# Kernel optimization log

Hardware: AMD Instinct MI355X
Metric: run time of the kernel (lower is better)

## Reference

```python
import jax, jax.numpy as jnp
import numpy as np
from jax import lax

B, S, MEL, DM, DI, N, K, R, H, V = 2, 2048, 80, 512, 1024, 16, 4, 32, 8, 10000


def setup_inputs() -> dict:
    ks = iter(jax.random.split(jax.random.key(0), 48))
    r = lambda sh, s=0.02: jax.random.normal(next(ks), sh, jnp.float32) * s
    inp = {"mel": jax.random.normal(next(ks), (B, S, MEL), jnp.float32)}
    inp["mel_w"] = r((DM, MEL)); inp["mel_b"] = r((DM,))
    inp["attn_in_w"] = r((3 * DM, DM)); inp["attn_in_b"] = r((3 * DM,))
    inp["attn_out_w"] = r((DM, DM)); inp["attn_out_b"] = r((DM,))
    inp["ln1_g"] = jnp.ones((DM,)); inp["ln1_b"] = jnp.zeros((DM,))
    inp["ln2_g"] = jnp.ones((DM,)); inp["ln2_b"] = jnp.zeros((DM,))
    for p in ("fm", "bm"):
        inp[p + "_in_w"] = r((2 * DI, DM))
        inp[p + "_conv_w"] = r((DI, K), 0.2)
        inp[p + "_conv_b"] = r((DI,), 0.1)
        inp[p + "_x_w"] = r((R + 2 * N, DI))
        inp[p + "_dt_w"] = r((DI, R), 0.1)
        inp[p + "_dt_b"] = r((DI,), 0.1)
        inp[p + "_A_log"] = jnp.log(jnp.tile(jnp.arange(1, N + 1, dtype=jnp.float32), (DI, 1)))
        inp[p + "_D"] = jnp.ones((DI,))
        inp[p + "_out_w"] = r((DM, DI))
    inp["bim_w"] = r((DM, 2 * DM)); inp["bim_b"] = r((DM,))
    inp["out_w"] = r((V, DM)); inp["out_b"] = r((V,))
    return inp


def _ln(x, g, b):
    mu = x.mean(-1, keepdims=True)
    var = ((x - mu) ** 2).mean(-1, keepdims=True)
    return (x - mu) * lax.rsqrt(var + 1e-5) * g + b


def _mha(x, in_w, in_b, out_w, out_b):
    # torch nn.MultiheadAttention default batch_first=False:
    # axis0 = sequence (here the batch dim B), axis1 = batch (here S). Faithful to source.
    L, Nb, E = x.shape
    hd = E // H
    qkv = x @ in_w.T + in_b
    q, k, v = jnp.split(qkv, 3, axis=-1)
    q = q.reshape(L, Nb, H, hd)
    k = k.reshape(L, Nb, H, hd)
    v = v.reshape(L, Nb, H, hd)
    sc = jnp.einsum('lnhd,mnhd->nhlm', q, k) / np.float32(np.sqrt(hd))
    a = jax.nn.softmax(sc, axis=-1)
    o = jnp.einsum('nhlm,mnhd->lnhd', a, v).reshape(L, Nb, E)
    return o @ out_w.T + out_b


def _mamba(x, in_w, conv_w, conv_b, x_w, dt_w, dt_b, A_log, Dp, out_w):
    # mamba_ssm Mamba block: in_proj -> causal depthwise conv + silu -> x_proj ->
    # softplus(dt_proj) -> selective scan -> gate by silu(z) -> out_proj
    Bb, L, _ = x.shape
    xa, z = jnp.split(x @ in_w.T, 2, axis=-1)  # [B,L,DI] each
    xc = lax.conv_general_dilated(xa.transpose(0, 2, 1), conv_w[:, None, :], (1,), [(K - 1, 0)],
                                  dimension_numbers=('NCH', 'OIH', 'NCH'), feature_group_count=DI)
    xc = jax.nn.silu(xc + conv_b[None, :, None]).transpose(0, 2, 1)  # [B,L,DI]
    dbl = xc @ x_w.T  # [B,L,R+2N]
    dt, Bm, Cm = dbl[..., :R], dbl[..., R:R + N], dbl[..., R + N:]
    dt = jax.nn.softplus(dt @ dt_w.T + dt_b)  # [B,L,DI]
    A = -jnp.exp(A_log)  # [DI,N]

    def step(h, ins):
        dt_t, B_t, C_t, x_t = ins  # [B,DI],[B,N],[B,N],[B,DI]
        h = jnp.exp(dt_t[..., None] * A) * h + (dt_t * x_t)[..., None] * B_t[:, None, :]
        return h, jnp.einsum('bdn,bn->bd', h, C_t)

    h0 = jnp.zeros((Bb, DI, N), x.dtype)
    _, ys = lax.scan(step, h0, (dt.transpose(1, 0, 2), Bm.transpose(1, 0, 2),
                                Cm.transpose(1, 0, 2), xc.transpose(1, 0, 2)))
    y = ys.transpose(1, 0, 2) + xc * Dp
    y = y * jax.nn.silu(z)
    return y @ out_w.T


def reference(mel, mel_w, mel_b, attn_in_w, attn_in_b, attn_out_w, attn_out_b,
              ln1_g, ln1_b, ln2_g, ln2_b,
              fm_in_w, fm_conv_w, fm_conv_b, fm_x_w, fm_dt_w, fm_dt_b, fm_A_log, fm_D, fm_out_w,
              bm_in_w, bm_conv_w, bm_conv_b, bm_x_w, bm_dt_w, bm_dt_b, bm_A_log, bm_D, bm_out_w,
              bim_w, bim_b, out_w, out_b):
    x = mel @ mel_w.T + mel_b  # [B,S,DM]
    x = _ln(x + _mha(x, attn_in_w, attn_in_b, attn_out_w, attn_out_b), ln1_g, ln1_b)
    fwd = _mamba(x, fm_in_w, fm_conv_w, fm_conv_b, fm_x_w, fm_dt_w, fm_dt_b, fm_A_log, fm_D, fm_out_w)
    bwd = jnp.flip(_mamba(jnp.flip(x, 1), bm_in_w, bm_conv_w, bm_conv_b, bm_x_w, bm_dt_w, bm_dt_b, bm_A_log, bm_D, bm_out_w), 1)
    m = jnp.concatenate([fwd, bwd], axis=-1) @ bim_w.T + bim_b
    x = _ln(x + m, ln2_g, ln2_b)
    return x @ out_w.T + out_b  # [B,S,V]
```

## Files before the change

kernel.cpp:

```cpp
#include <hip/hip_runtime.h>
#include <hip/hip_bf16.h>
#include <math.h>

#define SEQ 2048

typedef __attribute__((ext_vector_type(4))) float f32x4;
typedef __attribute__((ext_vector_type(2))) float f32x2;
typedef __attribute__((ext_vector_type(8))) short bf16x8s;
typedef __attribute__((ext_vector_type(8))) unsigned short ushort8;
typedef __attribute__((ext_vector_type(2))) unsigned int uint2v;

__device__ __forceinline__ short f2bf(float f) {
  union { float f; unsigned u; } c; c.f = f;
  unsigned u = c.u;
  u += 0x7fffu + ((u >> 16) & 1u);
  return (short)(u >> 16);
}
__device__ __forceinline__ float bf2f(unsigned short u) {
  union { unsigned u; float f; } c; c.u = ((unsigned)u) << 16; return c.f;
}

__device__ __forceinline__ void lds_load16(const void* g, void* s) {
  __builtin_amdgcn_global_load_lds(
      (const __attribute__((address_space(1))) void*)g,
      (__attribute__((address_space(3))) void*)s, 16, 0, 0);
}

template<int EPI, int OUTBF>
__launch_bounds__(256)
__global__ void gemm_bf16(const unsigned short* A, const unsigned short* B,
                          void* Cv, const float* __restrict__ bias,
                          int M, int N, int K, int lda, int ldb, int ldc, int nbn,
                          const unsigned short* A1, const unsigned short* B1, void* C1) {
  __shared__ char smem[67584];

  if (blockIdx.y) { A = A1; B = B1; Cv = C1; }

  const int nwg = gridDim.x;
  const int g = blockIdx.x;
  const int q = nwg >> 3, r = nwg & 7;
  const int xcd = g & 7, cidx = g >> 3;
  const int wg = (xcd < r ? xcd * (q + 1) : r * (q + 1) + (xcd - r) * q) + cidx;
  const int sup = nbn << 2;
  const int bmg = wg / sup, rem = wg % sup;
  const int bn = rem >> 2;
  const int bm = (bmg << 2) + (rem & 3);
  const int m0 = bm * 128, n0 = bn * 128;

  const int tid = threadIdx.x, lane = tid & 63, wave = tid >> 6;
  const int wr = (wave >> 1) * 64, wc = (wave & 1) * 64;
  const int fr = lane & 15, fq = lane >> 4;
  const int srow = tid >> 3;
  const int scc  = tid & 7;

  f32x4 acc[4][4] = {};
  const int nkt = K >> 6;

  auto STAGE = [&](int buf, int kt) {
    const int k0 = kt << 6;
    unsigned short* sAb = (unsigned short*)(smem + buf * 32768);
    unsigned short* sBb = (unsigned short*)(smem + buf * 32768 + 16384);
    #pragma unroll
    for (int j = 0; j < 4; j++) {
      int lrow = j * 32 + srow;
      int gcol = (scc ^ (lrow & 7)) * 8;
      lds_load16(A + (size_t)(m0 + lrow) * lda + k0 + gcol, &sAb[(j * 256 + wave * 64) * 8]);
    }
    #pragma unroll
    for (int j = 0; j < 4; j++) {
      int lrow = j * 32 + srow;
      int gcol = (scc ^ (lrow & 7)) * 8;
      int grow = n0 + lrow; if (grow >= N) grow = N - 1;
      lds_load16(B + (size_t)grow * ldb + k0 + gcol, &sBb[(j * 256 + wave * 64) * 8]);
    }
  };

  STAGE(0, 0);

  int cur = 0;
  for (int kt = 0; kt < nkt; kt++) {
    if (kt + 1 < nkt) {
      STAGE(cur ^ 1, kt + 1);
      asm volatile("s_waitcnt vmcnt(8)" ::: "memory");
    } else {
      asm volatile("s_waitcnt vmcnt(0)" ::: "memory");
    }
    __builtin_amdgcn_s_barrier();
    __builtin_amdgcn_sched_barrier(0);
    const unsigned short* As = (const unsigned short*)(smem + cur * 32768);
    const unsigned short* Bs = (const unsigned short*)(smem + cur * 32768 + 16384);
    #pragma unroll
    for (int ks = 0; ks < 2; ks++) {
      bf16x8s af[4], bfv[4];
      #pragma unroll
      for (int i = 0; i < 4; i++) {
        int ra = wr + i * 16 + fr;
        af[i] = *(const bf16x8s*)&As[ra * 64 + (((ks << 2) + fq) ^ (ra & 7)) * 8];
      }
      #pragma unroll
      for (int i = 0; i < 4; i++) {
        int rb = wc + i * 16 + fr;
        bfv[i] = *(const bf16x8s*)&Bs[rb * 64 + (((ks << 2) + fq) ^ (rb & 7)) * 8];
      }
      #pragma unroll
      for (int i = 0; i < 4; i++)
        #pragma unroll
        for (int j = 0; j < 4; j++)
          acc[i][j] = __builtin_amdgcn_mfma_f32_16x16x32_bf16(af[i], bfv[j], acc[i][j], 0, 0, 0);
    }
    __builtin_amdgcn_s_barrier();
    cur ^= 1;
  }

  float* ct = (float*)smem;
  #pragma unroll
  for (int i = 0; i < 4; i++)
    #pragma unroll
    for (int j = 0; j < 4; j++)
      #pragma unroll
      for (int r4 = 0; r4 < 4; r4++)
        ct[(wr + i * 16 + fq * 4 + r4) * 132 + wc + j * 16 + fr] = acc[i][j][r4];
  __syncthreads();
  const int half = lane >> 5;
  const int col4 = (lane & 31) * 4;
  const int cn = n0 + col4;
  #pragma unroll
  for (int it = 0; it < 16; it++) {
    int row = wave * 32 + it * 2 + half;
    f32x4 v = *(const f32x4*)&ct[row * 132 + col4];
    if (cn < N) {
      if (EPI >= 1) {
        f32x4 b4 = *(const f32x4*)&bias[cn];
        #pragma unroll
        for (int j = 0; j < 4; j++) v[j] += b4[j];
      }
      if (OUTBF) {
        unsigned short h0 = (unsigned short)f2bf(v[0]), h1 = (unsigned short)f2bf(v[1]);
        unsigned short h2 = (unsigned short)f2bf(v[2]), h3 = (unsigned short)f2bf(v[3]);
        uint2v o = { (unsigned)h0 | ((unsigned)h1 << 16), (unsigned)h2 | ((unsigned)h3 << 16) };
        *(uint2v*)((unsigned short*)Cv + (size_t)(m0 + row) * ldc + cn) = o;
      } else {
        float* dst = (float*)Cv + (size_t)(m0 + row) * ldc + cn;
        if (EPI == 1) __builtin_nontemporal_store(v, (f32x4*)dst);
        else          *(f32x4*)dst = v;
      }
    }
  }
}

__launch_bounds__(512)
__global__ void dt_kernel(const float* __restrict__ dbl0, const float* __restrict__ dtw0,
                          const float* __restrict__ dtb0, float* __restrict__ out0,
                          const float* __restrict__ dbl1, const float* __restrict__ dtw1,
                          const float* __restrict__ dtb1, float* __restrict__ out1) {
  const int dir = blockIdx.y;
  const float* dbl = dir ? dbl1 : dbl0;
  const float* dtw = dir ? dtw1 : dtw0;
  const float* dtb = dir ? dtb1 : dtb0;
  float* out = dir ? out1 : out0;
  const int t = threadIdx.x;
  const int d0 = t * 2;
  const int m0 = blockIdx.x * 16;
  float w0[32], w1[32];
  #pragma unroll
  for (int qq = 0; qq < 8; qq++) {
    f32x4 v0 = *(const f32x4*)(dtw + (size_t)d0 * 32 + qq * 4);
    f32x4 v1 = *(const f32x4*)(dtw + (size_t)(d0 + 1) * 32 + qq * 4);
    #pragma unroll
    for (int j = 0; j < 4; j++) { w0[qq * 4 + j] = v0[j]; w1[qq * 4 + j] = v1[j]; }
  }
  const float b0 = dtb[d0], b1 = dtb[d0 + 1];
  for (int mi = 0; mi < 16; mi++) {
    const float* dr = dbl + (size_t)(m0 + mi) * 64;
    float a0 = b0, a1 = b1;
    #pragma unroll
    for (int qq = 0; qq < 8; qq++) {
      f32x4 v = *(const f32x4*)(dr + qq * 4);
      #pragma unroll
      for (int j = 0; j < 4; j++) { a0 += v[j] * w0[qq * 4 + j]; a1 += v[j] * w1[qq * 4 + j]; }
    }
    a0 = fmaxf(a0, 0.f) + log1pf(__expf(-fabsf(a0)));
    a1 = fmaxf(a1, 0.f) + log1pf(__expf(-fabsf(a1)));
    f32x2 o = { a0, a1 };
    *(f32x2*)(out + (size_t)(m0 + mi) * 1024 + d0) = o;
  }
}

struct CvtArgs { const float* s[12]; unsigned short* d[12]; int n[12]; };
__global__ void cvt_many(CvtArgs a) {
  int y = blockIdx.y;
  int i = (blockIdx.x * 256 + threadIdx.x) * 8;
  if (i >= a.n[y]) return;
  const float* s = a.s[y];
  f32x4 v0 = *(const f32x4*)(s + i);
  f32x4 v1 = *(const f32x4*)(s + i + 4);
  ushort8 o = { (unsigned short)f2bf(v0[0]), (unsigned short)f2bf(v0[1]),
                (unsigned short)f2bf(v0[2]), (unsigned short)f2bf(v0[3]),
                (unsigned short)f2bf(v1[0]), (unsigned short)f2bf(v1[1]),
                (unsigned short)f2bf(v1[2]), (unsigned short)f2bf(v1[3]) };
  *(ushort8*)(a.d[y] + i) = o;
}

__global__ void cvt_pad(const float* __restrict__ s0, unsigned short* __restrict__ d0, int r0,
                        const float* __restrict__ s1, unsigned short* __restrict__ d1, int r1) {
  int y = blockIdx.y;
  const float* s = y ? s1 : s0;
  unsigned short* d = y ? d1 : d0;
  int rows = y ? r1 : r0;
  int idx = blockIdx.x * 256 + threadIdx.x;
  int c = idx & 15, row = idx >> 4;
  if (row >= rows) return;
  ushort8 o = { 0, 0, 0, 0, 0, 0, 0, 0 };
  if (c < 10) {
    f32x4 v0 = *(const f32x4*)(s + (size_t)row * 80 + c * 8);
    f32x4 v1 = *(const f32x4*)(s + (size_t)row * 80 + c * 8 + 4);
    o[0] = (unsigned short)f2bf(v0[0]); o[1] = (unsigned short)f2bf(v0[1]);
    o[2] = (unsigned short)f2bf(v0[2]); o[3] = (unsigned short)f2bf(v0[3]);
    o[4] = (unsigned short)f2bf(v1[0]); o[5] = (unsigned short)f2bf(v1[1]);
    o[6] = (unsigned short)f2bf(v1[2]); o[7] = (unsigned short)f2bf(v1[3]);
  }
  *(ushort8*)(d + (size_t)row * 128 + c * 8) = o;
}

__global__ void attn_kernel(const unsigned short* __restrict__ qkv, unsigned short* __restrict__ o) {
  int gw = blockIdx.x * 4 + (threadIdx.x >> 6);
  int lane = threadIdx.x & 63;
  int n = gw >> 3, h = gw & 7;
  size_t r0 = (size_t)n * 1536 + h * 64 + lane;
  size_t r1 = (size_t)(SEQ + n) * 1536 + h * 64 + lane;
  float q0 = bf2f(qkv[r0]), k0 = bf2f(qkv[r0 + 512]), v0 = bf2f(qkv[r0 + 1024]);
  float q1 = bf2f(qkv[r1]), k1 = bf2f(qkv[r1 + 512]), v1 = bf2f(qkv[r1 + 1024]);
  float s00 = q0 * k0, s01 = q0 * k1, s10 = q1 * k0, s11 = q1 * k1;
  #pragma unroll
  for (int off = 32; off > 0; off >>= 1) {
    s00 += __shfl_xor(s00, off);
    s01 += __shfl_xor(s01, off);
    s10 += __shfl_xor(s10, off);
    s11 += __shfl_xor(s11, off);
  }
  const float sc = 0.125f;
  s00 *= sc; s01 *= sc; s10 *= sc; s11 *= sc;
  float mx0 = fmaxf(s00, s01), mx1 = fmaxf(s10, s11);
  float e00 = __expf(s00 - mx0), e01 = __expf(s01 - mx0);
  float e10 = __expf(s10 - mx1), e11 = __expf(s11 - mx1);
  float i0 = 1.f / (e00 + e01), i1 = 1.f / (e10 + e11);
  size_t w0 = (size_t)n * 512 + h * 64 + lane;
  size_t w1 = (size_t)(SEQ + n) * 512 + h * 64 + lane;
  o[w0] = (unsigned short)f2bf((e00 * v0 + e01 * v1) * i0);
  o[w1] = (unsigned short)f2bf((e10 * v0 + e11 * v1) * i1);
}

template<int DUAL>
__global__ void ln_res_kernel(const unsigned short* __restrict__ a, const unsigned short* __restrict__ b,
                              const float* __restrict__ g, const float* __restrict__ be,
                              unsigned short* __restrict__ out, unsigned short* __restrict__ out2) {
  int row = blockIdx.x * 4 + (threadIdx.x >> 6);
  int lane = threadIdx.x & 63;
  ushort8 va = *(const ushort8*)(a + (size_t)row * 512 + lane * 8);
  ushort8 vb = *(const ushort8*)(b + (size_t)row * 512 + lane * 8);
  float v[8];
  #pragma unroll
  for (int j = 0; j < 8; j++) v[j] = bf2f(va[j]) + bf2f(vb[j]);
  float s = 0.f, s2 = 0.f;
  #pragma unroll
  for (int j = 0; j < 8; j++) { s += v[j]; s2 += v[j] * v[j]; }
  #pragma unroll
  for (int off = 32; off > 0; off >>= 1) { s += __shfl_xor(s, off); s2 += __shfl_xor(s2, off); }
  float mu = s * (1.f / 512.f);
  float var = s2 * (1.f / 512.f) - mu * mu;
  float rs = rsqrtf(var + 1e-5f);
  const float* pg = g + lane * 8;
  const float* pe = be + lane * 8;
  ushort8 o;
  #pragma unroll
  for (int j = 0; j < 8; j++) o[j] = (unsigned short)f2bf((v[j] - mu) * rs * pg[j] + pe[j]);
  *(ushort8*)(out + (size_t)row * 512 + lane * 8) = o;
  if (DUAL) {
    int t = row & (SEQ - 1), bb = row >> 11;
    int frow = (bb << 11) | (SEQ - 1 - t);
    *(ushort8*)(out2 + (size_t)frow * 512 + lane * 8) = o;
  }
}

struct ConvArgs {
  const unsigned short* xz[2];
  const float* w[2];
  const float* cb[2];
  unsigned short* xc[2];
};
__global__ void conv_silu_kernel(ConvArgs a) {
  int dir = blockIdx.y;
  int idx = blockIdx.x * 256 + threadIdx.x;
  int dc = (idx & 127) * 8;
  int t  = (idx >> 7) & (SEQ - 1);
  int b  = idx >> 18;
  const float* w = a.w[dir];
  f32x4 wv[8];
  #pragma unroll
  for (int j = 0; j < 8; j++) wv[j] = *(const f32x4*)(w + (dc + j) * 4);
  float acc[8];
  f32x4 cb0 = *(const f32x4*)(a.cb[dir] + dc), cb1 = *(const f32x4*)(a.cb[dir] + dc + 4);
  #pragma unroll
  for (int j = 0; j < 4; j++) { acc[j] = cb0[j]; acc[4 + j] = cb1[j]; }
  const unsigned short* base = a.xz[dir] + ((size_t)b * SEQ) * 2048 + dc;
  #pragma unroll
  for (int k = 0; k < 4; k++) {
    int tt = t - 3 + k;
    if (tt >= 0) {
      ushort8 xv = *(const ushort8*)(base + (size_t)tt * 2048);
      #pragma unroll
      for (int j = 0; j < 8; j++) acc[j] += wv[j][k] * bf2f(xv[j]);
    }
  }
  ushort8 o;
  #pragma unroll
  for (int j = 0; j < 8; j++) {
    float v = acc[j];
    o[j] = (unsigned short)f2bf(v / (1.f + __expf(-v)));
  }
  *(ushort8*)(a.xc[dir] + (size_t)idx * 8) = o;
}

#define CL 32
#define NC 64

struct ScanArgs {
  const unsigned short* xc[2];
  const float* dbl[2];
  const float* A_log[2];
  const float* dt[2];
  const float* Dp[2];
  const unsigned short* xz[2];
  float* hend[2];
  float* apr[2];
  float* h0[2];
  unsigned short* ys[2];
};

__global__ void scan_p1(ScanArgs s) {
  int dir = blockIdx.y;
  int tid = blockIdx.x * 256 + threadIdx.x;
  int nq = tid & 3;
  int d = (tid >> 2) & 1023;
  int c = (tid >> 12) & (NC - 1);
  int b = tid >> 18;
  f32x4 va = *(const f32x4*)(s.A_log[dir] + d * 16 + nq * 4);
  float A[4];
  #pragma unroll
  for (int j = 0; j < 4; j++) A[j] = -__expf(va[j]);
  float h[4] = {};
  float ap[4] = { 1.f, 1.f, 1.f, 1.f };
  const unsigned short* xcp = s.xc[dir] + ((size_t)b * SEQ) * 1024 + d;
  const float* dtp = s.dt[dir] + ((size_t)b * SEQ) * 1024 + d;
  const float* dbp = s.dbl[dir] + ((size_t)b * SEQ) * 64;
  const int t0 = c * CL;
  for (int t = t0; t < t0 + CL; t++) {
    float dtv = dtp[(size_t)t * 1024];
    float dx = dtv * bf2f(xcp[(size_t)t * 1024]);
    f32x4 Bv = *(const f32x4*)(dbp + (size_t)t * 64 + 32 + nq * 4);
    #pragma unroll
    for (int j = 0; j < 4; j++) {
      float e = __expf(dtv * A[j]);
      h[j] = e * h[j] + dx * Bv[j];
      ap[j] *= e;
    }
  }
  size_t o = ((size_t)((b * NC + c) * 1024 + d)) * 16 + nq * 4;
  f32x4 vh = { h[0], h[1], h[2], h[3] };
  f32x4 vap = { ap[0], ap[1], ap[2], ap[3] };
  *(f32x4*)(s.hend[dir] + o) = vh;
  *(f32x4*)(s.apr[dir] + o) = vap;
}

__global__ void scan_p2(ScanArgs s) {
  int dir = blockIdx.y;
  int tid = blockIdx.x * 256 + threadIdx.x;
  int n = tid & 15;
  int d = (tid >> 4) & 1023;
  int b = tid >> 14;
  const float* hend = s.hend[dir];
  const float* apr  = s.apr[dir];
  float* h0 = s.h0[dir];
  float h = 0.f;
  for (int c = 0; c < NC; c++) {
    size_t idx = ((size_t)((b * NC + c) * 1024 + d)) * 16 + n;
    h0[idx] = h;
    h = apr[idx] * h + hend[idx];
  }
}

__global__ void scan_p3(ScanArgs s) {
  int dir = blockIdx.y;
  int tid = blockIdx.x * 256 + threadIdx.x;
  int nq = tid & 3;
  int d = (tid >> 2) & 1023;
  int c = (tid >> 12) & (NC - 1);
  int b = tid >> 18;
  f32x4 va = *(const f32x4*)(s.A_log[dir] + d * 16 + nq * 4);
  float A[4];
  #pragma unroll
  for (int j = 0; j < 4; j++) A[j] = -__expf(va[j]);
  const float Dv = s.Dp[dir][d];
  size_t o = ((size_t)((b * NC + c) * 1024 + d)) * 16 + nq * 4;
  f32x4 h4 = *(const f32x4*)(s.h0[dir] + o);
  float h[4] = { h4[0], h4[1], h4[2], h4[3] };
  const unsigned short* xcp = s.xc[dir] + ((size_t)b * SEQ) * 1024 + d;
  const float* dtp = s.dt[dir] + ((size_t)b * SEQ) * 1024 + d;
  const unsigned short* zp  = s.xz[dir] + ((size_t)b * SEQ) * 2048 + 1024 + d;
  const float* dbp = s.dbl[dir] + ((size_t)b * SEQ) * 64;
  unsigned short* ysp = s.ys[dir] + ((size_t)b * SEQ) * 1024 + d;
  const int t0 = c * CL;
  for (int t = t0; t < t0 + CL; t++) {
    float dtv = dtp[(size_t)t * 1024];
    float xcv = bf2f(xcp[(size_t)t * 1024]);
    float dx = dtv * xcv;
    f32x4 Bv = *(const f32x4*)(dbp + (size_t)t * 64 + 32 + nq * 4);
    f32x4 Cv = *(const f32x4*)(dbp + (size_t)t * 64 + 48 + nq * 4);
    float y = 0.f;
    #pragma unroll
    for (int j = 0; j < 4; j++) {
      float e = __expf(dtv * A[j]);
      h[j] = e * h[j] + dx * Bv[j];
      y += h[j] * Cv[j];
    }
    y += __shfl_xor(y, 1);
    y += __shfl_xor(y, 2);
    if (nq == 0) {
      float z = bf2f(zp[(size_t)t * 2048]);
      float out = (y + xcv * Dv) * (z / (1.f + __expf(-z)));
      int tw = dir ? (SEQ - 1 - t) : t;
      ysp[(size_t)tw * 1024] = (unsigned short)f2bf(out);
    }
  }
}

extern "C" void kernel_launch(void* const* d_in, const int* in_sizes, int n_in,
                              void* d_out, int out_size, void* d_ws, size_t ws_size,
                              hipStream_t stream) {
  (void)in_sizes; (void)n_in; (void)out_size; (void)ws_size;
  const float* mel        = (const float*)d_in[0];
  const float* mel_w      = (const float*)d_in[1];
  const float* mel_b      = (const float*)d_in[2];
  const float* attn_in_b  = (const float*)d_in[4];
  const float* attn_out_b = (const float*)d_in[6];
  const float* ln1_g = (const float*)d_in[7];
  const float* ln1_b = (const float*)d_in[8];
  const float* ln2_g = (const float*)d_in[9];
  const float* ln2_b = (const float*)d_in[10];
  const float* bim_b = (const float*)d_in[30];
  const float* out_b = (const float*)d_in[32];

  char* wsb = (char*)d_ws;
  char* obb = (char*)d_out;

  unsigned short* w_attn_in  = (unsigned short*)(wsb + 0);
  unsigned short* w_attn_out = (unsigned short*)(wsb + 1572864);
  unsigned short* w_dir[2][4];
  for (int dir = 0; dir < 2; dir++) {
    size_t base = 2097152 + (size_t)dir * 3342336;
    w_dir[dir][0] = (unsigned short*)(wsb + base);
    w_dir[dir][1] = (unsigned short*)(wsb + base + 2097152);
    w_dir[dir][2] = (unsigned short*)(wsb + base + 2228224);
    w_dir[dir][3] = (unsigned short*)(wsb + base + 2293760);
  }
  unsigned short* w_bim = (unsigned short*)(wsb + 8781824);
  unsigned short* w_out = (unsigned short*)(wsb + 9830400);

  unsigned short* x0     = (unsigned short*)(wsb + 20971520);
  unsigned short* x1     = (unsigned short*)(wsb + 25165824);
  unsigned short* x1f    = (unsigned short*)(wsb + 29360128);
  unsigned short* attn_o = (unsigned short*)(wsb + 33554432);
  unsigned short* xc0    = (unsigned short*)(wsb + 37748736);
  unsigned short* ysb0   = (unsigned short*)(wsb + 46137344);
  unsigned short* mout   = (unsigned short*)(wsb + 62914560);
  unsigned short* minter = (unsigned short*)(wsb + 71303168);
  unsigned short* x2     = (unsigned short*)(wsb + 75497472);
  float*          dbl0   = (float*)(wsb + 79691776);
  unsigned short* melp   = (unsigned short*)(wsb + 80740352);
  unsigned short* melwp  = (unsigned short*)(wsb + 81788928);

  unsigned short* qkv  = (unsigned short*)(obb + 0);
  unsigned short* xz0  = (unsigned short*)(obb + 12582912);
  unsigned short* xz1  = (unsigned short*)(obb + 29360128);
  unsigned short* xc1  = (unsigned short*)(obb + 46137344);
  unsigned short* ysb1 = (unsigned short*)(obb + 54525952);
  float* hend0 = (float*)(obb + 62914560);
  float* hend1 = (float*)(obb + 71303168);
  float* apr0  = (float*)(obb + 79691776);
  float* apr1  = (float*)(obb + 88080384);
  float* h0s0  = (float*)(obb + 96468992);
  float* h0s1  = (float*)(obb + 104857600);
  float* dbl1  = (float*)(obb + 113246208);
  float* dtf0  = (float*)(obb + 114294784);
  float* dtf1  = (float*)(obb + 131072000);
  float* ob    = (float*)d_out;

  dim3 blk(256);

  {
    CvtArgs a;
    const float* srcs[12] = { (const float*)d_in[3], (const float*)d_in[5],
      (const float*)d_in[11], (const float*)d_in[14], (const float*)d_in[15], (const float*)d_in[19],
      (const float*)d_in[20], (const float*)d_in[23], (const float*)d_in[24], (const float*)d_in[28],
      (const float*)d_in[29], (const float*)d_in[31] };
    unsigned short* dsts[12] = { w_attn_in, w_attn_out,
      w_dir[0][0], w_dir[0][1], w_dir[0][2], w_dir[0][3],
      w_dir[1][0], w_dir[1][1], w_dir[1][2], w_dir[1][3],
      w_bim, w_out };
    int ns[12] = { 786432, 262144, 1048576, 65536, 32768, 524288,
                   1048576, 65536, 32768, 524288, 524288, 5120000 };
    for (int i = 0; i < 12; i++) { a.s[i] = srcs[i]; a.d[i] = dsts[i]; a.n[i] = ns[i]; }
    cvt_many<<<dim3(2500, 12), blk, 0, stream>>>(a);
    cvt_pad<<<dim3(256, 2), blk, 0, stream>>>(mel, melp, 4096, mel_w, melwp, 512);
  }

  gemm_bf16<1, 1><<<dim3(4 * 32), blk, 0, stream>>>(melp, melwp, x0, mel_b,
      4096, 512, 128, 128, 128, 512, 4, nullptr, nullptr, nullptr);
  gemm_bf16<1, 1><<<dim3(12 * 32), blk, 0, stream>>>(x0, w_attn_in, qkv, attn_in_b,
      4096, 1536, 512, 512, 512, 1536, 12, nullptr, nullptr, nullptr);
  attn_kernel<<<4096, blk, 0, stream>>>(qkv, attn_o);
  gemm_bf16<1, 1><<<dim3(4 * 32), blk, 0, stream>>>(attn_o, w_attn_out, qkv, attn_out_b,
      4096, 512, 512, 512, 512, 512, 4, nullptr, nullptr, nullptr);
  ln_res_kernel<1><<<1024, blk, 0, stream>>>(x0, qkv, ln1_g, ln1_b, x1, x1f);

  ScanArgs sa;
  ConvArgs ca;
  for (int dir = 0; dir < 2; dir++) {
    int base = 11 + dir * 9;
    ca.xz[dir] = dir ? xz1 : xz0;
    ca.w[dir]  = (const float*)d_in[base + 1];
    ca.cb[dir] = (const float*)d_in[base + 2];
    ca.xc[dir] = dir ? xc1 : xc0;
    sa.xc[dir]    = dir ? xc1 : xc0;
    sa.dbl[dir]   = dir ? dbl1 : dbl0;
    sa.A_log[dir] = (const float*)d_in[base + 6];
    sa.dt[dir]    = dir ? dtf1 : dtf0;
    sa.Dp[dir]    = (const float*)d_in[base + 7];
    sa.xz[dir]    = dir ? xz1 : xz0;
    sa.hend[dir]  = dir ? hend1 : hend0;
    sa.apr[dir]   = dir ? apr1 : apr0;
    sa.h0[dir]    = dir ? h0s1 : h0s0;
    sa.ys[dir]    = dir ? ysb1 : ysb0;
  }
  gemm_bf16<0, 1><<<dim3(16 * 32, 2), blk, 0, stream>>>(x1, w_dir[0][0], xz0, nullptr,
      4096, 2048, 512, 512, 512, 2048, 16, x1f, w_dir[1][0], xz1);
  conv_silu_kernel<<<dim3(2048, 2), blk, 0, stream>>>(ca);
  gemm_bf16<0, 0><<<dim3(1 * 32, 2), blk, 0, stream>>>(xc0, w_dir[0][1], dbl0, nullptr,
      4096, 64, 1024, 1024, 1024, 64, 1, xc1, w_dir[1][1], dbl1);
  dt_kernel<<<dim3(256, 2), dim3(512), 0, stream>>>(
      dbl0, (const float*)d_in[15], (const float*)d_in[16], dtf0,
      dbl1, (const float*)d_in[24], (const float*)d_in[25], dtf1);
  scan_p1<<<dim3(2048, 2), blk, 0, stream>>>(sa);
  scan_p2<<<dim3(128, 2), blk, 0, stream>>>(sa);
  scan_p3<<<dim3(2048, 2), blk, 0, stream>>>(sa);
  gemm_bf16<0, 1><<<dim3(4 * 32, 2), blk, 0, stream>>>(ysb0, w_dir[0][3], mout, nullptr,
      4096, 512, 1024, 1024, 1024, 1024, 4, ysb1, w_dir[1][3], mout + 512);

  gemm_bf16<1, 1><<<dim3(4 * 32), blk, 0, stream>>>(mout, w_bim, minter, bim_b,
      4096, 512, 1024, 1024, 1024, 512, 4, nullptr, nullptr, nullptr);
  ln_res_kernel<0><<<1024, blk, 0, stream>>>(x1, minter, ln2_g, ln2_b, x2, nullptr);
  gemm_bf16<1, 0><<<dim3(79 * 32), blk, 0, stream>>>(x2, w_out, ob, out_b,
      4096, 10000, 512, 512, 512, 10000, 79, nullptr, nullptr, nullptr);
}
```

Baseline: 353.9 us.

## Store dt in bf16, flip rows inside GEMM loads, merge conversion launches

The softplus dt output is now stored as bf16 instead of fp32, which halves the dt traffic read by both scan passes. The flipped copy of x1 that the layernorm used to write is dropped, and the backward-direction in_proj GEMM reverses row indices while loading A. The mel padding conversion is folded into the cvt_many launch, saving one kernel launch. An unroll pragma is added to the scan_p2 loop, and storing dt in bf16 costs some precision in the scan.

```diff
diff --git a/kernel.cpp b/kernel.cpp
--- a/kernel.cpp
+++ b/kernel.cpp
@@ -5,7 +5,6 @@
 #define SEQ 2048
 
 typedef __attribute__((ext_vector_type(4))) float f32x4;
-typedef __attribute__((ext_vector_type(2))) float f32x2;
 typedef __attribute__((ext_vector_type(8))) short bf16x8s;
 typedef __attribute__((ext_vector_type(8))) unsigned short ushort8;
 typedef __attribute__((ext_vector_type(2))) unsigned int uint2v;
@@ -26,7 +25,7 @@
       (__attribute__((address_space(3))) void*)s, 16, 0, 0);
 }
 
-template<int EPI, int OUTBF>
+template<int EPI, int OUTBF, int AFLIP1 = 0>
 __launch_bounds__(256)
 __global__ void gemm_bf16(const unsigned short* A, const unsigned short* B,
                           void* Cv, const float* __restrict__ bias,
@@ -35,6 +34,7 @@
   __shared__ char smem[67584];
 
   if (blockIdx.y) { A = A1; B = B1; Cv = C1; }
+  const bool aflip = AFLIP1 && blockIdx.y;
 
   const int nwg = gridDim.x;
   const int g = blockIdx.x;
@@ -64,7 +64,11 @@
     for (int j = 0; j < 4; j++) {
       int lrow = j * 32 + srow;
       int gcol = (scc ^ (lrow & 7)) * 8;
-      lds_load16(A + (size_t)(m0 + lrow) * lda + k0 + gcol, &sAb[(j * 256 + wave * 64) * 8]);
+      int arow = m0 + lrow;
+      if (AFLIP1) {
+        if (aflip) arow = (arow & ~(SEQ - 1)) | ((SEQ - 1) - (arow & (SEQ - 1)));
+      }
+      lds_load16(A + (size_t)arow * lda + k0 + gcol, &sAb[(j * 256 + wave * 64) * 8]);
     }
     #pragma unroll
     for (int j = 0; j < 4; j++) {
@@ -150,14 +154,14 @@
 
 __launch_bounds__(512)
 __global__ void dt_kernel(const float* __restrict__ dbl0, const float* __restrict__ dtw0,
-                          const float* __restrict__ dtb0, float* __restrict__ out0,
+                          const float* __restrict__ dtb0, unsigned short* __restrict__ out0,
                           const float* __restrict__ dbl1, const float* __restrict__ dtw1,
-                          const float* __restrict__ dtb1, float* __restrict__ out1) {
+                          const float* __restrict__ dtb1, unsigned short* __restrict__ out1) {
   const int dir = blockIdx.y;
   const float* dbl = dir ? dbl1 : dbl0;
   const float* dtw = dir ? dtw1 : dtw0;
   const float* dtb = dir ? dtb1 : dtb0;
-  float* out = dir ? out1 : out0;
+  unsigned short* out = dir ? out1 : out0;
   const int t = threadIdx.x;
   const int d0 = t * 2;
   const int m0 = blockIdx.x * 16;
@@ -181,14 +185,31 @@
     }
     a0 = fmaxf(a0, 0.f) + log1pf(__expf(-fabsf(a0)));
     a1 = fmaxf(a1, 0.f) + log1pf(__expf(-fabsf(a1)));
-    f32x2 o = { a0, a1 };
-    *(f32x2*)(out + (size_t)(m0 + mi) * 1024 + d0) = o;
-  }
-}
-
-struct CvtArgs { const float* s[12]; unsigned short* d[12]; int n[12]; };
+    unsigned pk = (unsigned)(unsigned short)f2bf(a0) | ((unsigned)(unsigned short)f2bf(a1) << 16);
+    *(unsigned*)(out + (size_t)(m0 + mi) * 1024 + d0) = pk;
+  }
+}
+
+struct CvtArgs { const float* s[14]; unsigned short* d[14]; int n[14]; int pad[14]; };
 __global__ void cvt_many(CvtArgs a) {
   int y = blockIdx.y;
+  if (a.pad[y]) {
+    int idx = blockIdx.x * 256 + threadIdx.x;
+    int c = idx & 15, row = idx >> 4;
+    if (row >= a.n[y]) return;
+    const float* s = a.s[y];
+    ushort8 o = { 0, 0, 0, 0, 0, 0, 0, 0 };
+    if (c < 10) {
+      f32x4 v0 = *(const f32x4*)(s + (size_t)row * 80 + c * 8);
+      f32x4 v1 = *(const f32x4*)(s + (size_t)row * 80 + c * 8 + 4);
+      o[0] = (unsigned short)f2bf(v0[0]); o[1] = (unsigned short)f2bf(v0[1]);
+      o[2] = (unsigned short)f2bf(v0[2]); o[3] = (unsigned short)f2bf(v0[3]);
+      o[4] = (unsigned short)f2bf(v1[0]); o[5] = (unsigned short)f2bf(v1[1]);
+      o[6] = (unsigned short)f2bf(v1[2]); o[7] = (unsigned short)f2bf(v1[3]);
+    }
+    *(ushort8*)(a.d[y] + (size_t)row * 128 + c * 8) = o;
+    return;
+  }
   int i = (blockIdx.x * 256 + threadIdx.x) * 8;
   if (i >= a.n[y]) return;
   const float* s = a.s[y];
@@ -201,27 +222,6 @@
   *(ushort8*)(a.d[y] + i) = o;
 }
 
-__global__ void cvt_pad(const float* __restrict__ s0, unsigned short* __restrict__ d0, int r0,
-                        const float* __restrict__ s1, unsigned short* __restrict__ d1, int r1) {
-  int y = blockIdx.y;
-  const float* s = y ? s1 : s0;
-  unsigned short* d = y ? d1 : d0;
-  int rows = y ? r1 : r0;
-  int idx = blockIdx.x * 256 + threadIdx.x;
-  int c = idx & 15, row = idx >> 4;
-  if (row >= rows) return;
-  ushort8 o = { 0, 0, 0, 0, 0, 0, 0, 0 };
-  if (c < 10) {
-    f32x4 v0 = *(const f32x4*)(s + (size_t)row * 80 + c * 8);
-    f32x4 v1 = *(const f32x4*)(s + (size_t)row * 80 + c * 8 + 4);
-    o[0] = (unsigned short)f2bf(v0[0]); o[1] = (unsigned short)f2bf(v0[1]);
-    o[2] = (unsigned short)f2bf(v0[2]); o[3] = (unsigned short)f2bf(v0[3]);
-    o[4] = (unsigned short)f2bf(v1[0]); o[5] = (unsigned short)f2bf(v1[1]);
-    o[6] = (unsigned short)f2bf(v1[2]); o[7] = (unsigned short)f2bf(v1[3]);
-  }
-  *(ushort8*)(d + (size_t)row * 128 + c * 8) = o;
-}
-
 __global__ void attn_kernel(const unsigned short* __restrict__ qkv, unsigned short* __restrict__ o) {
   int gw = blockIdx.x * 4 + (threadIdx.x >> 6);
   int lane = threadIdx.x & 63;
@@ -250,10 +250,9 @@
   o[w1] = (unsigned short)f2bf((e10 * v0 + e11 * v1) * i1);
 }
 
-template<int DUAL>
 __global__ void ln_res_kernel(const unsigned short* __restrict__ a, const unsigned short* __restrict__ b,
                               const float* __restrict__ g, const float* __restrict__ be,
-                              unsigned short* __restrict__ out, unsigned short* __restrict__ out2) {
+                              unsigned short* __restrict__ out) {
   int row = blockIdx.x * 4 + (threadIdx.x >> 6);
   int lane = threadIdx.x & 63;
   ushort8 va = *(const ushort8*)(a + (size_t)row * 512 + lane * 8);
@@ -275,11 +274,6 @@
   #pragma unroll
   for (int j = 0; j < 8; j++) o[j] = (unsigned short)f2bf((v[j] - mu) * rs * pg[j] + pe[j]);
   *(ushort8*)(out + (size_t)row * 512 + lane * 8) = o;
-  if (DUAL) {
-    int t = row & (SEQ - 1), bb = row >> 11;
-    int frow = (bb << 11) | (SEQ - 1 - t);
-    *(ushort8*)(out2 + (size_t)frow * 512 + lane * 8) = o;
-  }
 }
 
 struct ConvArgs {
@@ -328,7 +322,7 @@
   const unsigned short* xc[2];
   const float* dbl[2];
   const float* A_log[2];
-  const float* dt[2];
+  const unsigned short* dt[2];
   const float* Dp[2];
   const unsigned short* xz[2];
   float* hend[2];
@@ -351,11 +345,11 @@
   float h[4] = {};
   float ap[4] = { 1.f, 1.f, 1.f, 1.f };
   const unsigned short* xcp = s.xc[dir] + ((size_t)b * SEQ) * 1024 + d;
-  const float* dtp = s.dt[dir] + ((size_t)b * SEQ) * 1024 + d;
+  const unsigned short* dtp = s.dt[dir] + ((size_t)b * SEQ) * 1024 + d;
   const float* dbp = s.dbl[dir] + ((size_t)b * SEQ) * 64;
   const int t0 = c * CL;
   for (int t = t0; t < t0 + CL; t++) {
-    float dtv = dtp[(size_t)t * 1024];
+    float dtv = bf2f(dtp[(size_t)t * 1024]);
     float dx = dtv * bf2f(xcp[(size_t)t * 1024]);
     f32x4 Bv = *(const f32x4*)(dbp + (size_t)t * 64 + 32 + nq * 4);
     #pragma unroll
@@ -382,6 +376,7 @@
   const float* apr  = s.apr[dir];
   float* h0 = s.h0[dir];
   float h = 0.f;
+  #pragma unroll 8
   for (int c = 0; c < NC; c++) {
     size_t idx = ((size_t)((b * NC + c) * 1024 + d)) * 16 + n;
     h0[idx] = h;
@@ -405,13 +400,13 @@
   f32x4 h4 = *(const f32x4*)(s.h0[dir] + o);
   float h[4] = { h4[0], h4[1], h4[2], h4[3] };
   const unsigned short* xcp = s.xc[dir] + ((size_t)b * SEQ) * 1024 + d;
-  const float* dtp = s.dt[dir] + ((size_t)b * SEQ) * 1024 + d;
+  const unsigned short* dtp = s.dt[dir] + ((size_t)b * SEQ) * 1024 + d;
   const unsigned short* zp  = s.xz[dir] + ((size_t)b * SEQ) * 2048 + 1024 + d;
   const float* dbp = s.dbl[dir] + ((size_t)b * SEQ) * 64;
   unsigned short* ysp = s.ys[dir] + ((size_t)b * SEQ) * 1024 + d;
   const int t0 = c * CL;
   for (int t = t0; t < t0 + CL; t++) {
-    float dtv = dtp[(size_t)t * 1024];
+    float dtv = bf2f(dtp[(size_t)t * 1024]);
     float xcv = bf2f(xcp[(size_t)t * 1024]);
     float dx = dtv * xcv;
     f32x4 Bv = *(const f32x4*)(dbp + (size_t)t * 64 + 32 + nq * 4);
@@ -468,7 +463,6 @@
 
   unsigned short* x0     = (unsigned short*)(wsb + 20971520);
   unsigned short* x1     = (unsigned short*)(wsb + 25165824);
-  unsigned short* x1f    = (unsigned short*)(wsb + 29360128);
   unsigned short* attn_o = (unsigned short*)(wsb + 33554432);
   unsigned short* xc0    = (unsigned short*)(wsb + 37748736);
   unsigned short* ysb0   = (unsigned short*)(wsb + 46137344);
@@ -491,27 +485,27 @@
   float* h0s0  = (float*)(obb + 96468992);
   float* h0s1  = (float*)(obb + 104857600);
   float* dbl1  = (float*)(obb + 113246208);
-  float* dtf0  = (float*)(obb + 114294784);
-  float* dtf1  = (float*)(obb + 131072000);
+  unsigned short* dtf0 = (unsigned short*)(obb + 114294784);
+  unsigned short* dtf1 = (unsigned short*)(obb + 122683392);
   float* ob    = (float*)d_out;
 
   dim3 blk(256);
 
   {
     CvtArgs a;
-    const float* srcs[12] = { (const float*)d_in[3], (const float*)d_in[5],
+    const float* srcs[14] = { (const float*)d_in[3], (const float*)d_in[5],
       (const float*)d_in[11], (const float*)d_in[14], (const float*)d_in[15], (const float*)d_in[19],
       (const float*)d_in[20], (const float*)d_in[23], (const float*)d_in[24], (const float*)d_in[28],
-      (const float*)d_in[29], (const float*)d_in[31] };
-    unsigned short* dsts[12] = { w_attn_in, w_attn_out,
+      (const float*)d_in[29], (const float*)d_in[31], mel, mel_w };
+    unsigned short* dsts[14] = { w_attn_in, w_attn_out,
       w_dir[0][0], w_dir[0][1], w_dir[0][2], w_dir[0][3],
       w_dir[1][0], w_dir[1][1], w_dir[1][2], w_dir[1][3],
-      w_bim, w_out };
-    int ns[12] = { 786432, 262144, 1048576, 65536, 32768, 524288,
-                   1048576, 65536, 32768, 524288, 524288, 5120000 };
-    for (int i = 0; i < 12; i++) { a.s[i] = srcs[i]; a.d[i] = dsts[i]; a.n[i] = ns[i]; }
-    cvt_many<<<dim3(2500, 12), blk, 0, stream>>>(a);
-    cvt_pad<<<dim3(256, 2), blk, 0, stream>>>(mel, melp, 4096, mel_w, melwp, 512);
+      w_bim, w_out, melp, melwp };
+    int ns[14] = { 786432, 262144, 1048576, 65536, 32768, 524288,
+                   1048576, 65536, 32768, 524288, 524288, 5120000, 4096, 512 };
+    int pads[14] = { 0,0,0,0,0,0,0,0,0,0,0,0,1,1 };
+    for (int i = 0; i < 14; i++) { a.s[i] = srcs[i]; a.d[i] = dsts[i]; a.n[i] = ns[i]; a.pad[i] = pads[i]; }
+    cvt_many<<<dim3(2500, 14), blk, 0, stream>>>(a);
   }
 
   gemm_bf16<1, 1><<<dim3(4 * 32), blk, 0, stream>>>(melp, melwp, x0, mel_b,
@@ -521,7 +515,7 @@
   attn_kernel<<<4096, blk, 0, stream>>>(qkv, attn_o);
   gemm_bf16<1, 1><<<dim3(4 * 32), blk, 0, stream>>>(attn_o, w_attn_out, qkv, attn_out_b,
       4096, 512, 512, 512, 512, 512, 4, nullptr, nullptr, nullptr);
-  ln_res_kernel<1><<<1024, blk, 0, stream>>>(x0, qkv, ln1_g, ln1_b, x1, x1f);
+  ln_res_kernel<<<1024, blk, 0, stream>>>(x0, qkv, ln1_g, ln1_b, x1);
 
   ScanArgs sa;
   ConvArgs ca;
@@ -542,8 +536,8 @@
     sa.h0[dir]    = dir ? h0s1 : h0s0;
     sa.ys[dir]    = dir ? ysb1 : ysb0;
   }
-  gemm_bf16<0, 1><<<dim3(16 * 32, 2), blk, 0, stream>>>(x1, w_dir[0][0], xz0, nullptr,
-      4096, 2048, 512, 512, 512, 2048, 16, x1f, w_dir[1][0], xz1);
+  gemm_bf16<0, 1, 1><<<dim3(16 * 32, 2), blk, 0, stream>>>(x1, w_dir[0][0], xz0, nullptr,
+      4096, 2048, 512, 512, 512, 2048, 16, x1, w_dir[1][0], xz1);
   conv_silu_kernel<<<dim3(2048, 2), blk, 0, stream>>>(ca);
   gemm_bf16<0, 0><<<dim3(1 * 32, 2), blk, 0, stream>>>(xc0, w_dir[0][1], dbl0, nullptr,
       4096, 64, 1024, 1024, 1024, 64, 1, xc1, w_dir[1][1], dbl1);
@@ -558,7 +552,7 @@
 
   gemm_bf16<1, 1><<<dim3(4 * 32), blk, 0, stream>>>(mout, w_bim, minter, bim_b,
       4096, 512, 1024, 1024, 1024, 512, 4, nullptr, nullptr, nullptr);
-  ln_res_kernel<0><<<1024, blk, 0, stream>>>(x1, minter, ln2_g, ln2_b, x2, nullptr);
+  ln_res_kernel<<<1024, blk, 0, stream>>>(x1, minter, ln2_g, ln2_b, x2);
   gemm_bf16<1, 0><<<dim3(79 * 32), blk, 0, stream>>>(x2, w_out, ob, out_b,
       4096, 10000, 512, 512, 512, 10000, 79, nullptr, nullptr, nullptr);
 }
```

Result: no change. 359.3 us (+1.5%).
